# Optimization experiments

Hardware: AMD Instinct MI355X
Metric: run time of the kernel (lower is better)

The kernel has to match this reference:

```python
import jax, jax.numpy as jnp
import numpy as np

NEG_SLOPE = 0.2
N, E, NNZ, IN, H, C = 100000, 50000, 800000, 128, 8, 16


def setup_inputs() -> dict:
    key = jax.random.key(0)
    ks = jax.random.split(key, 8)
    X = jax.random.normal(ks[0], (N, IN), jnp.float32)
    W_typed = jax.random.normal(ks[1], (4, IN, H * C), jnp.float32) * (1.0 / np.sqrt(IN))
    att_e = jax.random.normal(ks[2], (4, H, C), jnp.float32) * 0.1
    att_v = jax.random.normal(ks[3], (4, H, C), jnp.float32) * 0.1
    vertex = jax.random.randint(ks[4], (NNZ,), 0, N, jnp.int32)
    edges = jax.random.randint(ks[5], (NNZ,), 0, E, jnp.int32)
    vtype = jax.random.randint(ks[6], (N,), 0, 4, jnp.int32)
    etype = jax.random.randint(ks[7], (E,), 0, 4, jnp.int32)
    return {"X": X, "W_typed": W_typed, "att_e": att_e, "att_v": att_v,
            "vertex": vertex, "edges": edges, "vtype": vtype, "etype": etype}


def _segment_softmax(logits, seg, num):
    # numerically-stable softmax over segments (PyG-style, eps in denominator)
    m = jax.ops.segment_max(logits, seg, num_segments=num)
    ex = jnp.exp(logits - m[seg])
    s = jax.ops.segment_sum(ex, seg, num_segments=num)
    return ex / (s[seg] + 1e-16)


def reference(X, W_typed, att_e, att_v, vertex, edges, vtype, etype):
    # typed linear: project with all 4 type weights, select per node type
    Xall = jnp.einsum('ni,tio->tno', X, W_typed)        # [4, N, H*C]
    X0 = Xall[vtype, jnp.arange(N)]                     # [N, H*C]
    Xn = X0.reshape(N, H, C)
    Xve = Xn[vertex]                                    # [NNZ, H, C] gather vertex->incidence
    # vertex->edge attention, typed by edge type of each incidence
    beta = jnp.sum(Xve * att_e[etype[edges]], axis=-1)  # [NNZ, H]
    beta = jax.nn.leaky_relu(beta, NEG_SLOPE)
    beta = _segment_softmax(beta, edges, E)
    Xe = jax.nn.relu(jax.ops.segment_sum(Xve * beta[..., None], edges, num_segments=E))  # [E, H, C]
    Xe = Xe[edges]                                      # [NNZ, H, C] gather edge->incidence
    # edge->vertex attention, typed by node type of each incidence's vertex
    alpha = jnp.sum(Xe * att_v[vtype[vertex]], axis=-1)  # [NNZ, H]
    alpha = jax.nn.leaky_relu(alpha, NEG_SLOPE)
    alpha = _segment_softmax(alpha, vertex, N)
    Xv = jax.ops.segment_sum(Xe * alpha[..., None], vertex, num_segments=N)  # [N, H, C]
    return Xv.reshape(N, H * C)
```

## Files before the change

kernel.cpp:

```cpp
#include <hip/hip_runtime.h>

typedef __attribute__((ext_vector_type(8))) short bf16x8;
typedef __attribute__((ext_vector_type(4))) float f32x4;

#define NEG_SLOPE 0.2f

__device__ __forceinline__ unsigned short f2bf(float f){
  unsigned u = __float_as_uint(f);
  u = (u + 0x7fffu + ((u >> 16) & 1u)) >> 16;
  return (unsigned short)u;
}
__device__ __forceinline__ float bflo(unsigned u){ return __uint_as_float(u << 16); }
__device__ __forceinline__ float bfhi(unsigned u){ return __uint_as_float(u & 0xffff0000u); }
__device__ __forceinline__ float lrelu(float x){ return x > 0.f ? x : NEG_SLOPE * x; }

__global__ __launch_bounds__(256) void k_prep(
    const int* __restrict__ vtype, int N, int* __restrict__ tcnt, int nbHN,
    const float* __restrict__ W, short* __restrict__ Bfrag){
  __shared__ int lcnt[4];
  int b = (int)blockIdx.x;
  if (b < nbHN){
    if (threadIdx.x < 4) lcnt[threadIdx.x] = 0;
    __syncthreads();
    int i = b * 256 + threadIdx.x;
    if (i < N) atomicAdd(&lcnt[vtype[i]], 1);
    __syncthreads();
    if (threadIdx.x < 4 && lcnt[threadIdx.x] > 0)
      atomicAdd(tcnt + threadIdx.x, lcnt[threadIdx.x]);
    return;
  }
  b -= nbHN;
  int u = b * 256 + threadIdx.x;
  int j = u & 7, lane = (u >> 3) & 63, ct = (u >> 9) & 31, ks = u >> 14;
  int k = ks * 32 + ((lane >> 4) << 3) + j;
  int col = (ct << 4) + (lane & 15);
  int t = col >> 7, o = col & 127;
  Bfrag[u] = (short)f2bf(W[(t * 128 + k) * 128 + o]);
}

__global__ void k_pbase(const int* __restrict__ tcnt, int* __restrict__ pbase){
  if (threadIdx.x == 0 && blockIdx.x == 0){
    int pb = 0;
    for (int t = 0; t < 4; ++t){
      pbase[t] = pb;
      pb += ((tcnt[t] + 63) >> 6) << 6;
    }
    pbase[4] = pb;
  }
}

__global__ __launch_bounds__(256) void k_nodeplace(
    const int* __restrict__ vtype, int N, const int* __restrict__ pbase,
    int* __restrict__ tcur, int* __restrict__ nsorted){
  __shared__ int lcnt[4];
  __shared__ int gbase[4];
  int t = threadIdx.x;
  if (t < 4) lcnt[t] = 0;
  __syncthreads();
  int i = (int)blockIdx.x * 256 + t;
  int tt = 0, rank = 0;
  bool valid = i < N;
  if (valid){ tt = vtype[i]; rank = atomicAdd(&lcnt[tt], 1); }
  __syncthreads();
  if (t < 4 && lcnt[t] > 0) gbase[t] = atomicAdd(tcur + t, lcnt[t]);
  __syncthreads();
  if (valid) nsorted[pbase[tt] + gbase[tt] + rank] = i;
}

__global__ __launch_bounds__(256, 3) void k_gemm_hist(const float* __restrict__ X,
    const short* __restrict__ Bfrag, const int* __restrict__ nsorted,
    const int* __restrict__ pbase, unsigned short* __restrict__ X0,
    const int* __restrict__ edges, int NNZ,
    int* __restrict__ cnt, int* __restrict__ rank_e, int nbHist){
  __shared__ short shB[8 * 4 * 64 * 8];
  const int tid = threadIdx.x;
  const int q = (int)blockIdx.x / 3, r = (int)blockIdx.x % 3;

  if (r != 0){
    int hb = 2 * q + (r - 1);
    if (hb < nbHist){
      int i = hb * 256 + tid;
      if (i < NNZ) rank_e[i] = atomicAdd(cnt + edges[i], 1);
    }
    return;
  }

  const int rowIdx = q * 64;
  const int t = (rowIdx >= pbase[1]) + (rowIdx >= pbase[2]) + (rowIdx >= pbase[3]);

  const bf16x8* Bv = (const bf16x8*)Bfrag;
  bf16x8* shBv = (bf16x8*)shB;
  #pragma unroll
  for (int v = 0; v < 8; ++v){
    int item = v * 256 + tid;
    int slab = item >> 6, ln = item & 63;
    int ks = slab >> 3, ctl = slab & 7;
    shBv[item] = Bv[((ks * 32 + 8 * t + ctl) * 64) + ln];
  }

  const int w = tid >> 6, lane = tid & 63;
  const int m = lane & 15, qq = lane >> 4;
  const int node = nsorted[rowIdx + w * 16 + m];

  bf16x8 afrag[4];
  #pragma unroll
  for (int ks = 0; ks < 4; ++ks){
    bf16x8 f;
    if (node >= 0){
      const float4* src = (const float4*)(X + (size_t)node * 128 + ks * 32 + qq * 8);
      float4 a = src[0], b = src[1];
      f[0]=(short)f2bf(a.x); f[1]=(short)f2bf(a.y); f[2]=(short)f2bf(a.z); f[3]=(short)f2bf(a.w);
      f[4]=(short)f2bf(b.x); f[5]=(short)f2bf(b.y); f[6]=(short)f2bf(b.z); f[7]=(short)f2bf(b.w);
    } else {
      #pragma unroll
      for (int z = 0; z < 8; ++z) f[z] = 0;
    }
    afrag[ks] = f;
  }

  f32x4 acc[8];
  #pragma unroll
  for (int ct = 0; ct < 8; ++ct){
    acc[ct][0]=0.f; acc[ct][1]=0.f; acc[ct][2]=0.f; acc[ct][3]=0.f;
  }

  __syncthreads();
  #pragma unroll
  for (int ctl = 0; ctl < 8; ++ctl){
    #pragma unroll
    for (int ks = 0; ks < 4; ++ks){
      bf16x8 bf = shBv[(ks * 8 + ctl) * 64 + lane];
      acc[ctl] = __builtin_amdgcn_mfma_f32_16x16x32_bf16(afrag[ks], bf, acc[ctl], 0, 0, 0);
    }
  }

  const int col0 = lane & 15;
  #pragma unroll
  for (int rr = 0; rr < 4; ++rr){
    int row = nsorted[rowIdx + w * 16 + qq * 4 + rr];
    if (row < 0) continue;
    #pragma unroll
    for (int ctl = 0; ctl < 8; ++ctl)
      X0[(size_t)row * 128 + ctl * 16 + col0] = f2bf(acc[ctl][rr]);
  }
}

__global__ __launch_bounds__(256) void k_scanA(const int* __restrict__ cnt, int S,
                                               int* __restrict__ bsum){
  __shared__ int sh[256];
  int base = blockIdx.x * 1024 + threadIdx.x * 4;
  int s = 0;
  #pragma unroll
  for (int k = 0; k < 4; ++k){ int idx = base + k; if (idx < S) s += cnt[idx]; }
  sh[threadIdx.x] = s; __syncthreads();
  for (int off = 128; off > 0; off >>= 1){
    if (threadIdx.x < off) sh[threadIdx.x] += sh[threadIdx.x + off];
    __syncthreads();
  }
  if (threadIdx.x == 0) bsum[blockIdx.x] = sh[0];
}

__global__ void k_scanB2(int* bsum, int nb){
  if (threadIdx.x == 0 && blockIdx.x == 0){
    int run = 0;
    for (int b = 0; b < nb; ++b){ int v = bsum[b]; bsum[b] = run; run += v; }
  }
}

__global__ __launch_bounds__(256) void k_scanC2(const int* __restrict__ cnt, int S,
    const int* __restrict__ bsum, int* __restrict__ offs){
  __shared__ int sh[256];
  int t = threadIdx.x;
  int b = (int)blockIdx.x;
  int base = b * 1024 + t * 4;
  int c[4]; int s = 0;
  #pragma unroll
  for (int k = 0; k < 4; ++k){ int idx = base + k; c[k] = (idx < S) ? cnt[idx] : 0; s += c[k]; }
  sh[t] = s; __syncthreads();
  for (int off = 1; off < 256; off <<= 1){
    int v = (t >= off) ? sh[t - off] : 0; __syncthreads();
    sh[t] += v; __syncthreads();
  }
  int run = bsum[b] + sh[t] - s;
  #pragma unroll
  for (int k = 0; k < 4; ++k){
    int idx = base + k;
    if (idx < S){ offs[idx] = run; run += c[k]; }
  }
}

__global__ __launch_bounds__(256) void k_place_e(
    const int* __restrict__ edges, const int* __restrict__ vertex, int NNZ,
    const int* __restrict__ offs, const int* __restrict__ rank_e,
    int* __restrict__ rows){
  int i = (int)blockIdx.x * 256 + (int)threadIdx.x;
  if (i < NNZ) rows[offs[edges[i]] + rank_e[i]] = vertex[i];
}

__global__ __launch_bounds__(256) void k_place_v(
    const int* __restrict__ edges, const int* __restrict__ vertex, int NNZ,
    const int* __restrict__ offsV, const int* __restrict__ rank_v,
    int* __restrict__ rowsV){
  int i = (int)blockIdx.x * 256 + (int)threadIdx.x;
  if (i < NNZ) rowsV[offsV[vertex[i]] + rank_v[i]] = edges[i];
}

template<int OUT_BF16>
__device__ __forceinline__ void seg_body(const uint4* __restrict__ feat,
    const float* __restrict__ att, const int* __restrict__ rows_sorted,
    const int* __restrict__ offs, const int* __restrict__ cnt,
    const int* __restrict__ stype, void* __restrict__ outbuf,
    int S, int blockId, int tid){
  int wid = tid >> 6, lane = tid & 63;
  int s = blockId * 4 + wid;
  if (s >= S) return;
  int t = stype[s];
  int sub = lane >> 4, lane16 = lane & 15;
  const float4* ap = (const float4*)(att + t * 128 + lane16 * 8);
  float4 A0 = ap[0], A1 = ap[1];
  int start = offs[s], len = cnt[s];
  float denom = 0.f;
  float acc[8];
  #pragma unroll
  for (int e = 0; e < 8; ++e) acc[e] = 0.f;

  for (int base = 0; base < len; base += 64){
    int m = len - base; if (m > 64) m = 64;
    int idx = 0;
    if (lane < m) idx = rows_sorted[start + base + lane];
    int ng = (m + 3) >> 2;
    uint4 uA = make_uint4(0,0,0,0), uB = make_uint4(0,0,0,0);
    {
      int r0 = __shfl(idx, sub);
      if (sub < m) uA = feat[(size_t)r0 * 16 + lane16];
      int r1 = __shfl(idx, 4 + sub);
      if (4 + sub < m) uB = feat[(size_t)r1 * 16 + lane16];
    }
    for (int g = 0; g < ng; g += 2){
      {
        uint4 u = uA;
        int nr = (g + 2) * 4 + sub;
        int rn = __shfl(idx, nr & 63);
        if (nr < m) uA = feat[(size_t)rn * 16 + lane16];
        float x0 = bflo(u.x), x1 = bfhi(u.x), x2 = bflo(u.y), x3 = bfhi(u.y);
        float x4 = bflo(u.z), x5 = bfhi(u.z), x6 = bflo(u.w), x7 = bfhi(u.w);
        float p = x0*A0.x + x1*A0.y + x2*A0.z + x3*A0.w
                + x4*A1.x + x5*A1.y + x6*A1.z + x7*A1.w;
        p += __shfl_xor(p, 1);
        float wgt = __expf(lrelu(p));
        wgt = (g * 4 + sub < m) ? wgt : 0.f;
        denom += wgt;
        acc[0] += wgt*x0; acc[1] += wgt*x1; acc[2] += wgt*x2; acc[3] += wgt*x3;
        acc[4] += wgt*x4; acc[5] += wgt*x5; acc[6] += wgt*x6; acc[7] += wgt*x7;
      }
      if (g + 1 < ng){
        uint4 u = uB;
        int nr = (g + 3) * 4 + sub;
        int rn = __shfl(idx, nr & 63);
        if (nr < m) uB = feat[(size_t)rn * 16 + lane16];
        float x0 = bflo(u.x), x1 = bfhi(u.x), x2 = bflo(u.y), x3 = bfhi(u.y);
        float x4 = bflo(u.z), x5 = bfhi(u.z), x6 = bflo(u.w), x7 = bfhi(u.w);
        float p = x0*A0.x + x1*A0.y + x2*A0.z + x3*A0.w
                + x4*A1.x + x5*A1.y + x6*A1.z + x7*A1.w;
        p += __shfl_xor(p, 1);
        float wgt = __expf(lrelu(p));
        wgt = ((g + 1) * 4 + sub < m) ? wgt : 0.f;
        denom += wgt;
        acc[0] += wgt*x0; acc[1] += wgt*x1; acc[2] += wgt*x2; acc[3] += wgt*x3;
        acc[4] += wgt*x4; acc[5] += wgt*x5; acc[6] += wgt*x6; acc[7] += wgt*x7;
      }
    }
  }
  denom += __shfl_xor(denom, 16);
  denom += __shfl_xor(denom, 32);
  #pragma unroll
  for (int e = 0; e < 8; ++e){
    acc[e] += __shfl_xor(acc[e], 16);
    acc[e] += __shfl_xor(acc[e], 32);
  }
  float inv = 1.f / (denom + 1e-16f);
  float v[8];
  #pragma unroll
  for (int e = 0; e < 8; ++e) v[e] = acc[e] * inv;

  if constexpr (OUT_BF16){
    if (sub == 0){
      uint4 pw;
      pw.x = (unsigned)f2bf(fmaxf(v[0],0.f)) | ((unsigned)f2bf(fmaxf(v[1],0.f)) << 16);
      pw.y = (unsigned)f2bf(fmaxf(v[2],0.f)) | ((unsigned)f2bf(fmaxf(v[3],0.f)) << 16);
      pw.z = (unsigned)f2bf(fmaxf(v[4],0.f)) | ((unsigned)f2bf(fmaxf(v[5],0.f)) << 16);
      pw.w = (unsigned)f2bf(fmaxf(v[6],0.f)) | ((unsigned)f2bf(fmaxf(v[7],0.f)) << 16);
      ((uint4*)outbuf)[(size_t)s * 16 + lane16] = pw;
    }
  } else {
    if (sub == 0){
      float4* op = (float4*)outbuf;
      op[(size_t)s * 32 + lane16 * 2]     = make_float4(v[0], v[1], v[2], v[3]);
      op[(size_t)s * 32 + lane16 * 2 + 1] = make_float4(v[4], v[5], v[6], v[7]);
    }
  }
}

__global__ __launch_bounds__(256) void k_seg1_histv(
    const int* __restrict__ vertex, int NNZ,
    int* __restrict__ cntV, int* __restrict__ rank_v, int nbHist,
    const uint4* __restrict__ X0, const float* __restrict__ att_e,
    const int* __restrict__ rows, const int* __restrict__ offs,
    const int* __restrict__ cnt, const int* __restrict__ etype,
    void* __restrict__ Xe, int E, int nbSeg){
  const int q = (int)blockIdx.x / 5, r = (int)blockIdx.x % 5;
  if (r == 0){
    if (q < nbHist){
      int i = q * 256 + (int)threadIdx.x;
      if (i < NNZ) rank_v[i] = atomicAdd(cntV + vertex[i], 1);
    }
    return;
  }
  int segBlk = q * 4 + (r - 1);
  if (segBlk >= nbSeg) return;
  seg_body<1>(X0, att_e, rows, offs, cnt, etype, Xe, E, segBlk, threadIdx.x);
}

__global__ __launch_bounds__(256) void k_seg2(const uint4* __restrict__ Xe,
    const float* __restrict__ att_v, const int* __restrict__ rows,
    const int* __restrict__ offs, const int* __restrict__ cnt,
    const int* __restrict__ vtype, float* __restrict__ out, int N){
  seg_body<0>(Xe, att_v, rows, offs, cnt, vtype, out, N,
              (int)blockIdx.x, threadIdx.x);
}

extern "C" void kernel_launch(void* const* d_in, const int* in_sizes, int n_in,
                              void* d_out, int out_size, void* d_ws, size_t ws_size,
                              hipStream_t stream){
  const float* X      = (const float*)d_in[0];
  const float* W      = (const float*)d_in[1];
  const float* att_e  = (const float*)d_in[2];
  const float* att_v  = (const float*)d_in[3];
  const int*   vertex = (const int*)d_in[4];
  const int*   edges  = (const int*)d_in[5];
  const int*   vtype  = (const int*)d_in[6];
  const int*   etype  = (const int*)d_in[7];
  float* out = (float*)d_out;
  const int N   = in_sizes[0] / 128;
  const int NNZ = in_sizes[4];
  const int E   = in_sizes[7];
  const int S   = E + N;

  const int nbI = (NNZ + 255) / 256;
  const int nbHN = (N + 255) / 256;
  const int nbSE = (E + 1023) / 1024;
  const int nbSV = (N + 1023) / 1024;
  const int nbSeg1 = (E + 3) / 4;
  const int nbPad = (N + 252 + 63) / 64;
  const int nsortedCap = nbPad * 64;
  const int nQA = (nbPad > (nbI + 1) / 2) ? nbPad : (nbI + 1) / 2;
  const int nQB = (nbI > (nbSeg1 + 3) / 4) ? nbI : (nbSeg1 + 3) / 4;

  char* wp = (char*)d_ws;
  int* cnt    = (int*)wp; wp += (size_t)S * 4;
  int* tcnt   = (int*)wp; wp += 16;
  int* tcur   = (int*)wp; wp += 16;
  int* offs   = (int*)wp; wp += (size_t)S * 4;
  int* bsum   = (int*)wp; wp += 1024;
  int* pbase  = (int*)wp; wp += 32;
  int* rows   = (int*)wp; wp += (size_t)2 * NNZ * 4;
  int* nsorted= (int*)wp; wp += (size_t)nsortedCap * 4;
  int* rank_e = (int*)wp; wp += (size_t)NNZ * 4;
  int* rank_v = (int*)wp; wp += (size_t)NNZ * 4;
  unsigned short* X0 = (unsigned short*)wp; wp += (size_t)N * 128 * 2;
  unsigned short* Xe = (unsigned short*)wp; wp += (size_t)E * 128 * 2;
  short* Bfrag = (short*)wp; wp += (size_t)65536 * 2;

  hipMemsetAsync(cnt, 0, (size_t)(S + 8) * 4, stream);
  hipMemsetAsync(nsorted, 0xFF, (size_t)nsortedCap * 4, stream);

  k_prep<<<nbHN + 256, 256, 0, stream>>>(vtype, N, tcnt, nbHN, W, Bfrag);
  k_pbase<<<1, 64, 0, stream>>>(tcnt, pbase);
  k_nodeplace<<<nbHN, 256, 0, stream>>>(vtype, N, pbase, tcur, nsorted);

  k_gemm_hist<<<3 * nQA, 256, 0, stream>>>(X, Bfrag, nsorted, pbase,
      (unsigned short*)X0, edges, NNZ, cnt, rank_e, nbI);

  k_scanA<<<nbSE, 256, 0, stream>>>(cnt, E, bsum);
  k_scanB2<<<1, 64, 0, stream>>>(bsum, nbSE);
  k_scanC2<<<nbSE, 256, 0, stream>>>(cnt, E, bsum, offs);
  k_place_e<<<nbI, 256, 0, stream>>>(edges, vertex, NNZ, offs, rank_e, rows);

  k_seg1_histv<<<5 * nQB, 256, 0, stream>>>(vertex, NNZ, cnt + E, rank_v, nbI,
      (const uint4*)X0, att_e, rows, offs, cnt, etype, Xe, E, nbSeg1);

  k_scanA<<<nbSV, 256, 0, stream>>>(cnt + E, N, bsum);
  k_scanB2<<<1, 64, 0, stream>>>(bsum, nbSV);
  k_scanC2<<<nbSV, 256, 0, stream>>>(cnt + E, N, bsum, offs + E);
  k_place_v<<<nbI, 256, 0, stream>>>(edges, vertex, NNZ, offs + E, rank_v,
      rows + NNZ);

  k_seg2<<<(N + 3) / 4, 256, 0, stream>>>((const uint4*)Xe, att_v,
      rows + NNZ, offs + E, cnt + E, vtype, out, N);
}
```

Measured before the change: 320.0 us.

## Deepen gather prefetch, fold block-sum scan into scan kernel, batch histogram atomics

The segment softmax body now keeps four rows in flight per lane group instead of two, which deepens the gather prefetch to hide more memory latency at the cost of extra registers. The single-thread block-sum scan kernel is removed, and each scan block instead redoes a small shared-memory scan of the block sums. This saves two launches and a serial pass. The histogram side-blocks each handle four times as many incidences, which shrinks the grid when the histogram side dominates the block count.

```diff
diff --git a/kernel.cpp b/kernel.cpp
--- a/kernel.cpp
+++ b/kernel.cpp
@@ -71,16 +71,20 @@
     const short* __restrict__ Bfrag, const int* __restrict__ nsorted,
     const int* __restrict__ pbase, unsigned short* __restrict__ X0,
     const int* __restrict__ edges, int NNZ,
-    int* __restrict__ cnt, int* __restrict__ rank_e, int nbHist){
+    int* __restrict__ cnt, int* __restrict__ rank_e, int nbHist4){
   __shared__ short shB[8 * 4 * 64 * 8];
   const int tid = threadIdx.x;
   const int q = (int)blockIdx.x / 3, r = (int)blockIdx.x % 3;
 
   if (r != 0){
     int hb = 2 * q + (r - 1);
-    if (hb < nbHist){
-      int i = hb * 256 + tid;
-      if (i < NNZ) rank_e[i] = atomicAdd(cnt + edges[i], 1);
+    if (hb < nbHist4){
+      int i0 = hb * 1024 + tid;
+      #pragma unroll
+      for (int k = 0; k < 4; ++k){
+        int i = i0 + k * 256;
+        if (i < NNZ) rank_e[i] = atomicAdd(cnt + edges[i], 1);
+      }
     }
     return;
   }
@@ -160,18 +164,19 @@
   if (threadIdx.x == 0) bsum[blockIdx.x] = sh[0];
 }
 
-__global__ void k_scanB2(int* bsum, int nb){
-  if (threadIdx.x == 0 && blockIdx.x == 0){
-    int run = 0;
-    for (int b = 0; b < nb; ++b){ int v = bsum[b]; bsum[b] = run; run += v; }
-  }
-}
-
-__global__ __launch_bounds__(256) void k_scanC2(const int* __restrict__ cnt, int S,
-    const int* __restrict__ bsum, int* __restrict__ offs){
+__global__ __launch_bounds__(256) void k_scanC3(const int* __restrict__ cnt, int S,
+    const int* __restrict__ bsum, int nb, int* __restrict__ offs){
+  __shared__ int shb[256];
   __shared__ int sh[256];
   int t = threadIdx.x;
   int b = (int)blockIdx.x;
+  shb[t] = (t < nb) ? bsum[t] : 0;
+  __syncthreads();
+  for (int off = 1; off < 256; off <<= 1){
+    int v = (t >= off) ? shb[t - off] : 0; __syncthreads();
+    shb[t] += v; __syncthreads();
+  }
+  int bbase = (b == 0) ? 0 : shb[b - 1];
   int base = b * 1024 + t * 4;
   int c[4]; int s = 0;
   #pragma unroll
@@ -181,7 +186,7 @@
     int v = (t >= off) ? sh[t - off] : 0; __syncthreads();
     sh[t] += v; __syncthreads();
   }
-  int run = bsum[b] + sh[t] - s;
+  int run = bbase + sh[t] - s;
   #pragma unroll
   for (int k = 0; k < 4; ++k){
     int idx = base + k;
@@ -204,6 +209,20 @@
   int i = (int)blockIdx.x * 256 + (int)threadIdx.x;
   if (i < NNZ) rowsV[offsV[vertex[i]] + rank_v[i]] = edges[i];
 }
+
+#define SEG_PROC(u, ROWPOS)                                                   \
+  {                                                                           \
+    float x0=bflo((u).x), x1=bfhi((u).x), x2=bflo((u).y), x3=bfhi((u).y);     \
+    float x4=bflo((u).z), x5=bfhi((u).z), x6=bflo((u).w), x7=bfhi((u).w);     \
+    float p = x0*A0.x + x1*A0.y + x2*A0.z + x3*A0.w                           \
+            + x4*A1.x + x5*A1.y + x6*A1.z + x7*A1.w;                          \
+    p += __shfl_xor(p, 1);                                                    \
+    float wgt = __expf(lrelu(p));                                             \
+    wgt = ((ROWPOS) < m) ? wgt : 0.f;                                         \
+    denom += wgt;                                                             \
+    acc[0]+=wgt*x0; acc[1]+=wgt*x1; acc[2]+=wgt*x2; acc[3]+=wgt*x3;           \
+    acc[4]+=wgt*x4; acc[5]+=wgt*x5; acc[6]+=wgt*x6; acc[7]+=wgt*x7;           \
+  }
 
 template<int OUT_BF16>
 __device__ __forceinline__ void seg_body(const uint4* __restrict__ feat,
@@ -230,44 +249,37 @@
     if (lane < m) idx = rows_sorted[start + base + lane];
     int ng = (m + 3) >> 2;
     uint4 uA = make_uint4(0,0,0,0), uB = make_uint4(0,0,0,0);
+    uint4 uC = make_uint4(0,0,0,0), uD = make_uint4(0,0,0,0);
     {
-      int r0 = __shfl(idx, sub);
-      if (sub < m) uA = feat[(size_t)r0 * 16 + lane16];
-      int r1 = __shfl(idx, 4 + sub);
-      if (4 + sub < m) uB = feat[(size_t)r1 * 16 + lane16];
-    }
-    for (int g = 0; g < ng; g += 2){
+      int r0 = __shfl(idx, sub);        if (sub < m)      uA = feat[(size_t)r0 * 16 + lane16];
+      int r1 = __shfl(idx, 4 + sub);    if (4 + sub < m)  uB = feat[(size_t)r1 * 16 + lane16];
+      int r2 = __shfl(idx, 8 + sub);    if (8 + sub < m)  uC = feat[(size_t)r2 * 16 + lane16];
+      int r3 = __shfl(idx, 12 + sub);   if (12 + sub < m) uD = feat[(size_t)r3 * 16 + lane16];
+    }
+    for (int g = 0; g < ng; g += 4){
       {
-        uint4 u = uA;
-        int nr = (g + 2) * 4 + sub;
+        uint4 u = uA; int nr = (g + 4) * 4 + sub;
         int rn = __shfl(idx, nr & 63);
         if (nr < m) uA = feat[(size_t)rn * 16 + lane16];
-        float x0 = bflo(u.x), x1 = bfhi(u.x), x2 = bflo(u.y), x3 = bfhi(u.y);
-        float x4 = bflo(u.z), x5 = bfhi(u.z), x6 = bflo(u.w), x7 = bfhi(u.w);
-        float p = x0*A0.x + x1*A0.y + x2*A0.z + x3*A0.w
-                + x4*A1.x + x5*A1.y + x6*A1.z + x7*A1.w;
-        p += __shfl_xor(p, 1);
-        float wgt = __expf(lrelu(p));
-        wgt = (g * 4 + sub < m) ? wgt : 0.f;
-        denom += wgt;
-        acc[0] += wgt*x0; acc[1] += wgt*x1; acc[2] += wgt*x2; acc[3] += wgt*x3;
-        acc[4] += wgt*x4; acc[5] += wgt*x5; acc[6] += wgt*x6; acc[7] += wgt*x7;
+        SEG_PROC(u, g * 4 + sub)
       }
       if (g + 1 < ng){
-        uint4 u = uB;
-        int nr = (g + 3) * 4 + sub;
+        uint4 u = uB; int nr = (g + 5) * 4 + sub;
         int rn = __shfl(idx, nr & 63);
         if (nr < m) uB = feat[(size_t)rn * 16 + lane16];
-        float x0 = bflo(u.x), x1 = bfhi(u.x), x2 = bflo(u.y), x3 = bfhi(u.y);
-        float x4 = bflo(u.z), x5 = bfhi(u.z), x6 = bflo(u.w), x7 = bfhi(u.w);
-        float p = x0*A0.x + x1*A0.y + x2*A0.z + x3*A0.w
-                + x4*A1.x + x5*A1.y + x6*A1.z + x7*A1.w;
-        p += __shfl_xor(p, 1);
-        float wgt = __expf(lrelu(p));
-        wgt = ((g + 1) * 4 + sub < m) ? wgt : 0.f;
-        denom += wgt;
-        acc[0] += wgt*x0; acc[1] += wgt*x1; acc[2] += wgt*x2; acc[3] += wgt*x3;
-        acc[4] += wgt*x4; acc[5] += wgt*x5; acc[6] += wgt*x6; acc[7] += wgt*x7;
+        SEG_PROC(u, (g + 1) * 4 + sub)
+      }
+      if (g + 2 < ng){
+        uint4 u = uC; int nr = (g + 6) * 4 + sub;
+        int rn = __shfl(idx, nr & 63);
+        if (nr < m) uC = feat[(size_t)rn * 16 + lane16];
+        SEG_PROC(u, (g + 2) * 4 + sub)
+      }
+      if (g + 3 < ng){
+        uint4 u = uD; int nr = (g + 7) * 4 + sub;
+        int rn = __shfl(idx, nr & 63);
+        if (nr < m) uD = feat[(size_t)rn * 16 + lane16];
+        SEG_PROC(u, (g + 3) * 4 + sub)
       }
     }
   }
@@ -300,19 +312,24 @@
     }
   }
 }
+#undef SEG_PROC
 
 __global__ __launch_bounds__(256) void k_seg1_histv(
     const int* __restrict__ vertex, int NNZ,
-    int* __restrict__ cntV, int* __restrict__ rank_v, int nbHist,
+    int* __restrict__ cntV, int* __restrict__ rank_v, int nbHist4,
     const uint4* __restrict__ X0, const float* __restrict__ att_e,
     const int* __restrict__ rows, const int* __restrict__ offs,
     const int* __restrict__ cnt, const int* __restrict__ etype,
     void* __restrict__ Xe, int E, int nbSeg){
   const int q = (int)blockIdx.x / 5, r = (int)blockIdx.x % 5;
   if (r == 0){
-    if (q < nbHist){
-      int i = q * 256 + (int)threadIdx.x;
-      if (i < NNZ) rank_v[i] = atomicAdd(cntV + vertex[i], 1);
+    if (q < nbHist4){
+      int i0 = q * 1024 + (int)threadIdx.x;
+      #pragma unroll
+      for (int k = 0; k < 4; ++k){
+        int i = i0 + k * 256;
+        if (i < NNZ) rank_v[i] = atomicAdd(cntV + vertex[i], 1);
+      }
     }
     return;
   }
@@ -347,14 +364,15 @@
   const int S   = E + N;
 
   const int nbI = (NNZ + 255) / 256;
+  const int nbH4 = (NNZ + 1023) / 1024;
   const int nbHN = (N + 255) / 256;
   const int nbSE = (E + 1023) / 1024;
   const int nbSV = (N + 1023) / 1024;
   const int nbSeg1 = (E + 3) / 4;
   const int nbPad = (N + 252 + 63) / 64;
   const int nsortedCap = nbPad * 64;
-  const int nQA = (nbPad > (nbI + 1) / 2) ? nbPad : (nbI + 1) / 2;
-  const int nQB = (nbI > (nbSeg1 + 3) / 4) ? nbI : (nbSeg1 + 3) / 4;
+  const int nQA = (nbPad > (nbH4 + 1) / 2) ? nbPad : (nbH4 + 1) / 2;
+  const int nQB = (nbH4 > (nbSeg1 + 3) / 4) ? nbH4 : (nbSeg1 + 3) / 4;
 
   char* wp = (char*)d_ws;
   int* cnt    = (int*)wp; wp += (size_t)S * 4;
@@ -379,19 +397,17 @@
   k_nodeplace<<<nbHN, 256, 0, stream>>>(vtype, N, pbase, tcur, nsorted);
 
   k_gemm_hist<<<3 * nQA, 256, 0, stream>>>(X, Bfrag, nsorted, pbase,
-      (unsigned short*)X0, edges, NNZ, cnt, rank_e, nbI);
+      (unsigned short*)X0, edges, NNZ, cnt, rank_e, nbH4);
 
   k_scanA<<<nbSE, 256, 0, stream>>>(cnt, E, bsum);
-  k_scanB2<<<1, 64, 0, stream>>>(bsum, nbSE);
-  k_scanC2<<<nbSE, 256, 0, stream>>>(cnt, E, bsum, offs);
+  k_scanC3<<<nbSE, 256, 0, stream>>>(cnt, E, bsum, nbSE, offs);
   k_place_e<<<nbI, 256, 0, stream>>>(edges, vertex, NNZ, offs, rank_e, rows);
 
-  k_seg1_histv<<<5 * nQB, 256, 0, stream>>>(vertex, NNZ, cnt + E, rank_v, nbI,
+  k_seg1_histv<<<5 * nQB, 256, 0, stream>>>(vertex, NNZ, cnt + E, rank_v, nbH4,
       (const uint4*)X0, att_e, rows, offs, cnt, etype, Xe, E, nbSeg1);
 
   k_scanA<<<nbSV, 256, 0, stream>>>(cnt + E, N, bsum);
-  k_scanB2<<<1, 64, 0, stream>>>(bsum, nbSV);
-  k_scanC2<<<nbSV, 256, 0, stream>>>(cnt + E, N, bsum, offs + E);
+  k_scanC3<<<nbSV, 256, 0, stream>>>(cnt + E, N, bsum, nbSV, offs + E);
   k_place_v<<<nbI, 256, 0, stream>>>(edges, vertex, NNZ, offs + E, rank_v,
       rows + NNZ);
 
```

New measurement: 327.7 us. 1.02x slower.
